# Kernel tuning notes

Measured on AMD Instinct MI355X. Metric: run time of the kernel, lower is better.

Reference implementation:

```python
import jax, jax.numpy as jnp
import numpy as np
import math

DIM = 1024
NUM_HEADS = 16
HEAD_DIM = DIM // NUM_HEADS
MAX_SEQ_LEN = 2048


def setup_inputs() -> dict:
    key = jax.random.key(0)
    ks = jax.random.split(key, 10)
    B, S = 4, 2048
    std = 1.0 / math.sqrt(DIM)
    inp = {
        "x": jax.random.normal(ks[0], (B, S, DIM), dtype=jnp.float32),
        "key_padding_mask": jnp.zeros((B, S), dtype=jnp.bool_),
        "q_w": jax.random.uniform(ks[1], (DIM, DIM), minval=-std, maxval=std),
        "q_b": jax.random.uniform(ks[2], (DIM,), minval=-std, maxval=std),
        "k_w": jax.random.uniform(ks[3], (DIM, DIM), minval=-std, maxval=std),
        "k_b": jax.random.uniform(ks[4], (DIM,), minval=-std, maxval=std),
        "v_w": jax.random.uniform(ks[5], (DIM, DIM), minval=-std, maxval=std),
        "v_b": jax.random.uniform(ks[6], (DIM,), minval=-std, maxval=std),
        "o_w": jax.random.uniform(ks[7], (DIM, DIM), minval=-std, maxval=std),
        "o_b": jax.random.uniform(ks[8], (DIM,), minval=-std, maxval=std),
    }
    return inp


def _rope_tables(seq_len):
    # freqs over half the head dim, per the RotaryPositionalEmbedding module
    half = HEAD_DIM // 2
    freqs = 1.0 / (10000.0 ** (jnp.arange(0, HEAD_DIM, 2, dtype=jnp.float32) / HEAD_DIM))
    pos = jnp.arange(seq_len, dtype=jnp.float32)
    ang = jnp.outer(pos, freqs)  # [S, half]
    return jnp.cos(ang)[:, :half], jnp.sin(ang)[:, :half]


def _apply_rope(t, cos, sin):
    # t: [B, H, S, D]; rotate first/second halves (non-interleaved variant)
    half = HEAD_DIM // 2
    left, right = t[..., :half], t[..., half:]
    return jnp.concatenate([left * cos - right * sin,
                            left * sin + right * cos], axis=-1)


def reference(x, key_padding_mask, q_w, q_b, k_w, k_b, v_w, v_b, o_w, o_b):
    B, S, _ = x.shape
    scale = HEAD_DIM ** -0.5

    def proj(w, b):
        y = jnp.einsum('bsd,ed->bse', x, w) + b  # torch Linear: x @ W^T + b
        return y.reshape(B, S, NUM_HEADS, HEAD_DIM).transpose(0, 2, 1, 3)

    q = proj(q_w, q_b)  # [B, H, S, D]
    k = proj(k_w, k_b)
    v = proj(v_w, v_b)

    cos, sin = _rope_tables(S)  # [S, half], broadcast over B,H
    q = _apply_rope(q, cos, sin)
    k = _apply_rope(k, cos, sin)

    scores = jnp.einsum('bhqd,bhkd->bhqk', q, k) * scale
    scores = jnp.where(key_padding_mask[:, None, None, :], -1e9, scores)
    weights = jax.nn.softmax(scores, axis=-1)  # dropout p=0.0 -> identity
    out = jnp.einsum('bhqk,bhkd->bhqd', weights, v)
    out = out.transpose(0, 2, 1, 3).reshape(B, S, DIM)
    return jnp.einsum('bsd,ed->bse', out, o_w) + o_b
```

## Files before the change

### kernel.cpp

```cpp
#include <hip/hip_runtime.h>
#include <stdint.h>

#define SEQ   2048
#define BATCH 4
#define NH    16
#define HD    64
#define DIMN  1024
#define MROWS (BATCH*SEQ)

typedef __attribute__((ext_vector_type(8))) short          bf16x8;
typedef __attribute__((ext_vector_type(8))) unsigned short ushort8;
typedef __attribute__((ext_vector_type(4))) float          f32x4;

static __device__ __forceinline__ unsigned short f2bf(float f) {
    unsigned int u = __builtin_bit_cast(unsigned int, f);
    u += 0x7fffu + ((u >> 16) & 1u);
    return (unsigned short)(u >> 16);
}
static __device__ __forceinline__ unsigned int pack2bf(float lo, float hi) {
    unsigned int a = __builtin_bit_cast(unsigned int, lo) + 0x8000u;
    unsigned int b = __builtin_bit_cast(unsigned int, hi) + 0x8000u;
    return __builtin_amdgcn_perm(b, a, 0x07060302u);
}
static __device__ __forceinline__ unsigned int pack2bf_trunc(float lo, float hi) {
    return __builtin_amdgcn_perm(__builtin_bit_cast(unsigned int, hi),
                                 __builtin_bit_cast(unsigned int, lo), 0x07060302u);
}

__global__ __launch_bounds__(256) void prologue_kernel(
        const float* __restrict__ x,
        const float* __restrict__ qw, const float* __restrict__ kw,
        const float* __restrict__ vw, const float* __restrict__ ow,
        unsigned short* __restrict__ xb,
        unsigned short* __restrict__ wq, unsigned short* __restrict__ wk,
        unsigned short* __restrict__ wv, unsigned short* __restrict__ wo,
        float* __restrict__ cosT, float* __restrict__ sinT,
        const unsigned char* __restrict__ mask, unsigned long long* __restrict__ m64) {
    const int bx = blockIdx.x, tid = threadIdx.x;
    if (bx < 4096 + 2048) {
        const float* s; unsigned short* d; int i;
        if (bx < 4096) { s = x; d = xb; i = bx * 2048 + tid * 8; }
        else {
            int wb = bx - 4096;
            int wsel = wb >> 9;
            s = wsel == 0 ? qw : (wsel == 1 ? kw : (wsel == 2 ? vw : ow));
            d = wsel == 0 ? wq : (wsel == 1 ? wk : (wsel == 2 ? wv : wo));
            i = (wb & 511) * 2048 + tid * 8;
        }
        float4 a = *(const float4*)(s + i);
        float4 b = *(const float4*)(s + i + 4);
        ushort8 o;
        o[0]=f2bf(a.x); o[1]=f2bf(a.y); o[2]=f2bf(a.z); o[3]=f2bf(a.w);
        o[4]=f2bf(b.x); o[5]=f2bf(b.y); o[6]=f2bf(b.z); o[7]=f2bf(b.w);
        *(ushort8*)(d + i) = o;
    } else if (bx < 6400) {
        int idx = (bx - 6144) * 256 + tid;
        int s = idx >> 5, j = idx & 31;
        float t = (float)(2 * j) / 64.0f;
        float freq = 1.0f / powf(10000.0f, t);
        float ang  = (float)s * freq;
        cosT[idx] = cosf(ang);
        sinT[idx] = sinf(ang);
    } else {
        if (tid < 128) {
            int b = tid >> 5, kt = tid & 31;
            const unsigned char* p = mask + b * SEQ + kt * 64;
            unsigned long long v = 0;
            for (int j = 0; j < 64; j++) v |= (unsigned long long)(p[j] != 0) << j;
            m64[tid] = v;
        }
    }
}

__global__ __launch_bounds__(256) void gemm_qkvt(const unsigned short* __restrict__ X,
        const unsigned short* __restrict__ Wq, const unsigned short* __restrict__ Wk,
        const unsigned short* __restrict__ Wv,
        const float* __restrict__ bq, const float* __restrict__ bk, const float* __restrict__ bv,
        unsigned short* __restrict__ Qo, unsigned short* __restrict__ Ko, unsigned short* __restrict__ Vto,
        const float* __restrict__ cosT, const float* __restrict__ sinT) {
    __shared__ __align__(16) unsigned short As[128 * 32];
    __shared__ __align__(16) unsigned short Bs[128 * 32];
    const int which = blockIdx.x >> 3;
    const int tid  = threadIdx.x;
    const int wid  = tid >> 6, lane = tid & 63;
    const int quad = lane >> 4, l15 = lane & 15;
    const int wm   = wid >> 1,  wn  = wid & 1;

    const unsigned short *Ag, *Bg;
    int m0, n0;
    if (which < 2) {
        m0 = blockIdx.y * 128;
        n0 = (blockIdx.x & 7) * 128;
        Ag = X;  Bg = which == 0 ? Wq : Wk;
    } else {
        m0 = (blockIdx.x & 7) * 128;
        n0 = blockIdx.y * 128;
        Ag = Wv; Bg = X;
    }

    f32x4 acc[4][4];
#pragma unroll
    for (int i = 0; i < 4; i++)
#pragma unroll
        for (int j = 0; j < 4; j++) acc[i][j] = (f32x4)0.0f;

    const int rb = wid * 32 + (lane >> 2);
    const int cb = (((lane & 3) ^ ((lane >> 3) & 3)) * 8);
    const int rq = (quad ^ ((l15 >> 1) & 3)) * 8;

    for (int k0 = 0; k0 < DIMN; k0 += 32) {
#pragma unroll
        for (int i = 0; i < 2; i++) {
            const unsigned short* ga = Ag + (size_t)(m0 + rb + i * 16) * DIMN + k0 + cb;
            __builtin_amdgcn_global_load_lds((const __attribute__((address_space(1))) void*)ga,
                (__attribute__((address_space(3))) void*)&As[(wid * 32 + i * 16) * 32], 16, 0, 0);
            const unsigned short* gb = Bg + (size_t)(n0 + rb + i * 16) * DIMN + k0 + cb;
            __builtin_amdgcn_global_load_lds((const __attribute__((address_space(1))) void*)gb,
                (__attribute__((address_space(3))) void*)&Bs[(wid * 32 + i * 16) * 32], 16, 0, 0);
        }
        __syncthreads();
        bf16x8 af[4], bfr[4];
#pragma unroll
        for (int f = 0; f < 4; f++) af[f]  = *(const bf16x8*)&As[(wm * 64 + f * 16 + l15) * 32 + rq];
#pragma unroll
        for (int f = 0; f < 4; f++) bfr[f] = *(const bf16x8*)&Bs[(wn * 64 + f * 16 + l15) * 32 + rq];
#pragma unroll
        for (int fm = 0; fm < 4; fm++)
#pragma unroll
            for (int fn = 0; fn < 4; fn++)
                acc[fm][fn] = __builtin_amdgcn_mfma_f32_16x16x32_bf16(af[fm], bfr[fn], acc[fm][fn], 0, 0, 0);
        __syncthreads();
    }

    if (which < 2) {
        const float* bias   = which == 0 ? bq : bk;
        unsigned short* Out = which == 0 ? Qo : Ko;
        const float scale = which == 0 ? 0.18033688011112042f : 1.0f;
        float bv4[4];
#pragma unroll
        for (int fn = 0; fn < 4; fn++) bv4[fn] = bias[n0 + wn * 64 + fn * 16 + l15];
        const int h = (n0 >> 6) + wn;
#pragma unroll
        for (int fm = 0; fm < 4; fm++)
#pragma unroll
            for (int r = 0; r < 4; r++) {
                int mrow = m0 + wm * 64 + fm * 16 + quad * 4 + r;
                int b = mrow >> 11, s = mrow & (SEQ - 1);
                unsigned short* orow = Out + ((size_t)(b * NH + h) * SEQ + s) * HD;
                float v0 = (acc[fm][0][r] + bv4[0]) * scale;
                float v1 = (acc[fm][1][r] + bv4[1]) * scale;
                float v2 = (acc[fm][2][r] + bv4[2]) * scale;
                float v3 = (acc[fm][3][r] + bv4[3]) * scale;
                int d0 = l15, d1 = 16 + l15;
                float c0 = cosT[s * 32 + d0], s0 = sinT[s * 32 + d0];
                float c1 = cosT[s * 32 + d1], s1 = sinT[s * 32 + d1];
                orow[d0]      = f2bf(v0 * c0 - v2 * s0);
                orow[d0 + 32] = f2bf(v0 * s0 + v2 * c0);
                orow[d1]      = f2bf(v1 * c1 - v3 * s1);
                orow[d1 + 32] = f2bf(v1 * s1 + v3 * c1);
            }
    } else {
        float4 bb[4];
#pragma unroll
        for (int fm = 0; fm < 4; fm++)
            bb[fm] = *(const float4*)&bv[m0 + wm * 64 + fm * 16 + quad * 4];
        const int b     = n0 >> 11;
        const int sbase = (n0 & (SEQ - 1)) + wn * 64 + l15;
#pragma unroll
        for (int fm = 0; fm < 4; fm++)
#pragma unroll
            for (int r = 0; r < 4; r++) {
                int e = m0 + wm * 64 + fm * 16 + quad * 4 + r;
                float bval = r == 0 ? bb[fm].x : (r == 1 ? bb[fm].y : (r == 2 ? bb[fm].z : bb[fm].w));
                unsigned short* row = Vto + ((size_t)(b * NH + (e >> 6)) * HD + (e & 63)) * SEQ + sbase;
#pragma unroll
                for (int fn = 0; fn < 4; fn++)
                    row[fn * 16] = f2bf(acc[fm][fn][r] + bval);
            }
    }
}

__global__ __launch_bounds__(256) void gemm_bt(const unsigned short* __restrict__ A,
                                               const unsigned short* __restrict__ W,
                                               const float* __restrict__ bias,
                                               float* __restrict__ out) {
    __shared__ __align__(16) unsigned short As[128 * 32];
    __shared__ __align__(16) unsigned short Bs[128 * 32];
    const int tid  = threadIdx.x;
    const int wid  = tid >> 6, lane = tid & 63;
    const int quad = lane >> 4, l15 = lane & 15;
    const int wm   = wid >> 1,  wn  = wid & 1;
    const int m0   = blockIdx.y * 128, n0 = blockIdx.x * 128;

    f32x4 acc[4][4];
#pragma unroll
    for (int i = 0; i < 4; i++)
#pragma unroll
        for (int j = 0; j < 4; j++) acc[i][j] = (f32x4)0.0f;

    const int rb = wid * 32 + (lane >> 2);
    const int cb = (((lane & 3) ^ ((lane >> 3) & 3)) * 8);
    const int rq = (quad ^ ((l15 >> 1) & 3)) * 8;

    for (int k0 = 0; k0 < DIMN; k0 += 32) {
#pragma unroll
        for (int i = 0; i < 2; i++) {
            const unsigned short* ga = A + (size_t)(m0 + rb + i * 16) * DIMN + k0 + cb;
            __builtin_amdgcn_global_load_lds((const __attribute__((address_space(1))) void*)ga,
                (__attribute__((address_space(3))) void*)&As[(wid * 32 + i * 16) * 32], 16, 0, 0);
            const unsigned short* gb = W + (size_t)(n0 + rb + i * 16) * DIMN + k0 + cb;
            __builtin_amdgcn_global_load_lds((const __attribute__((address_space(1))) void*)gb,
                (__attribute__((address_space(3))) void*)&Bs[(wid * 32 + i * 16) * 32], 16, 0, 0);
        }
        __syncthreads();
        bf16x8 af[4], bfr[4];
#pragma unroll
        for (int f = 0; f < 4; f++) af[f]  = *(const bf16x8*)&As[(wm * 64 + f * 16 + l15) * 32 + rq];
#pragma unroll
        for (int f = 0; f < 4; f++) bfr[f] = *(const bf16x8*)&Bs[(wn * 64 + f * 16 + l15) * 32 + rq];
#pragma unroll
        for (int fm = 0; fm < 4; fm++)
#pragma unroll
            for (int fn = 0; fn < 4; fn++)
                acc[fm][fn] = __builtin_amdgcn_mfma_f32_16x16x32_bf16(af[fm], bfr[fn], acc[fm][fn], 0, 0, 0);
        __syncthreads();
    }

    float bv4[4];
#pragma unroll
    for (int fn = 0; fn < 4; fn++) bv4[fn] = bias[n0 + wn * 64 + fn * 16 + l15];
#pragma unroll
    for (int fm = 0; fm < 4; fm++)
#pragma unroll
        for (int r = 0; r < 4; r++) {
            int mrow = m0 + wm * 64 + fm * 16 + quad * 4 + r;
            float* orow = out + (size_t)mrow * DIMN + n0 + wn * 64;
#pragma unroll
            for (int fn = 0; fn < 4; fn++) orow[fn * 16 + l15] = acc[fm][fn][r] + bv4[fn];
        }
}

#define PSTRIDE 36
__global__ __launch_bounds__(256, 4) void attn_kernel(const unsigned short* __restrict__ Q,
                                                      const unsigned short* __restrict__ K,
                                                      const unsigned short* __restrict__ Vt,
                                                      const unsigned long long* __restrict__ M64,
                                                      unsigned short* __restrict__ Ob) {
    __shared__ __align__(16) unsigned short Ks[8 * 512];
    __shared__ __align__(16) unsigned short Vs[8 * 512];
    __shared__ __align__(16) unsigned short Ps[4 * 64 * PSTRIDE];

    const int tid  = threadIdx.x;
    const int wid  = tid >> 6, lane = tid & 63;
    const int quad = lane >> 4, l15 = lane & 15;
    const int bid = blockIdx.x;
    const int bh  = (bid & 7) * 8 + (bid >> 7);
    const int qt  = (bid >> 3) & 15;
    const int b = bh >> 4, h = bh & 15;
    const int q0 = qt * 128;

    bf16x8 qf[2][2];
#pragma unroll
    for (int n = 0; n < 2; n++) {
        const int qs = q0 + wid * 32 + n * 16 + l15;
#pragma unroll
        for (int dk = 0; dk < 2; dk++)
            qf[n][dk] = __builtin_bit_cast(bf16x8,
                *(const uint4*)&Q[((size_t)bh * SEQ + qs) * HD + dk * 32 + quad * 8]);
    }

    f32x4 Oa[4][2];
#pragma unroll
    for (int i = 0; i < 4; i++)
#pragma unroll
        for (int n = 0; n < 2; n++) Oa[i][n] = (f32x4)0.0f;
    float ls[2] = {0.0f, 0.0f};

    unsigned short* Pw = &Ps[wid * 64 * PSTRIDE];
    const unsigned long long* Mrow = M64 + b * (SEQ / 64);

    const int s0 = wid * 2, s1 = s0 + 1;
    const unsigned short* Kg = K + (size_t)bh * SEQ * HD;
    const unsigned short* Vg = Vt + (size_t)bh * HD * SEQ;
    const unsigned short* gk0 = Kg + (size_t)((s0 >> 1) * 16 + l15) * HD + (s0 & 1) * 32 + quad * 8;
    const unsigned short* gk1 = Kg + (size_t)((s1 >> 1) * 16 + l15) * HD + (s1 & 1) * 32 + quad * 8;
    const unsigned short* gv0 = Vg + (size_t)((s0 >> 1) * 16 + l15) * SEQ + (s0 & 1) * 32 + quad * 8;
    const unsigned short* gv1 = Vg + (size_t)((s1 >> 1) * 16 + l15) * SEQ + (s1 & 1) * 32 + quad * 8;

    for (int kt = 0; kt < SEQ / 64; kt++) {
        const int k0 = kt * 64;
        __builtin_amdgcn_global_load_lds(
            (const __attribute__((address_space(1))) void*)(gk0 + (size_t)k0 * HD),
            (__attribute__((address_space(3))) void*)&Ks[s0 * 512], 16, 0, 0);
        __builtin_amdgcn_global_load_lds(
            (const __attribute__((address_space(1))) void*)(gk1 + (size_t)k0 * HD),
            (__attribute__((address_space(3))) void*)&Ks[s1 * 512], 16, 0, 0);
        __builtin_amdgcn_global_load_lds(
            (const __attribute__((address_space(1))) void*)(gv0 + k0),
            (__attribute__((address_space(3))) void*)&Vs[s0 * 512], 16, 0, 0);
        __builtin_amdgcn_global_load_lds(
            (const __attribute__((address_space(1))) void*)(gv1 + k0),
            (__attribute__((address_space(3))) void*)&Vs[s1 * 512], 16, 0, 0);
        unsigned long long mb = Mrow[kt];
        __syncthreads();

#pragma unroll
        for (int h2 = 0; h2 < 2; h2++) {
            bf16x8 kf[2][2];
#pragma unroll
            for (int f2 = 0; f2 < 2; f2++)
#pragma unroll
                for (int dk = 0; dk < 2; dk++)
                    kf[f2][dk] = *(const bf16x8*)&Ks[(((h2 * 2 + f2) << 1) + dk) * 512 + lane * 8];
            bf16x8 vf[4];
#pragma unroll
            for (int df = 0; df < 4; df++)
                vf[df] = *(const bf16x8*)&Vs[((df << 1) + h2) * 512 + lane * 8];

            f32x4 st[2][2];
            __builtin_amdgcn_s_setprio(1);
#pragma unroll
            for (int f2 = 0; f2 < 2; f2++)
#pragma unroll
                for (int n = 0; n < 2; n++) {
                    st[f2][n] = __builtin_amdgcn_mfma_f32_16x16x32_bf16(kf[f2][0], qf[n][0], (f32x4)0.0f, 0, 0, 0);
                    st[f2][n] = __builtin_amdgcn_mfma_f32_16x16x32_bf16(kf[f2][1], qf[n][1], st[f2][n], 0, 0, 0);
                }
            __builtin_amdgcn_s_setprio(0);

            unsigned int mh = (unsigned int)(mb >> (h2 * 32));
            if (mh) {
#pragma unroll
                for (int f2 = 0; f2 < 2; f2++)
#pragma unroll
                    for (int n = 0; n < 2; n++)
#pragma unroll
                        for (int r = 0; r < 4; r++) {
                            int kk = f2 * 16 + quad * 4 + r;
                            if ((mh >> kk) & 1u) st[f2][n][r] = -1e9f;
                        }
            }

#pragma unroll
            for (int f2 = 0; f2 < 2; f2++)
#pragma unroll
                for (int n = 0; n < 2; n++) {
                    float p0 = __builtin_amdgcn_exp2f(st[f2][n][0]);
                    float p1 = __builtin_amdgcn_exp2f(st[f2][n][1]);
                    float p2 = __builtin_amdgcn_exp2f(st[f2][n][2]);
                    float p3 = __builtin_amdgcn_exp2f(st[f2][n][3]);
                    ls[n] += (p0 + p1) + (p2 + p3);
                    uint2 w;
                    w.x = pack2bf_trunc(p0, p1);
                    w.y = pack2bf_trunc(p2, p3);
                    *(uint2*)&Pw[(h2 * 32 + n * 16 + l15) * PSTRIDE + f2 * 16 + quad * 4] = w;
                }
            bf16x8 pf[2];
#pragma unroll
            for (int n = 0; n < 2; n++) {
                uint2 plo = *(const uint2*)&Pw[(h2 * 32 + n * 16 + l15) * PSTRIDE + quad * 8];
                uint2 phi = *(const uint2*)&Pw[(h2 * 32 + n * 16 + l15) * PSTRIDE + quad * 8 + 4];
                uint4 pw4;
                pw4.x = plo.x; pw4.y = plo.y; pw4.z = phi.x; pw4.w = phi.y;
                pf[n] = __builtin_bit_cast(bf16x8, pw4);
            }
            __builtin_amdgcn_s_setprio(1);
#pragma unroll
            for (int df = 0; df < 4; df++)
#pragma unroll
                for (int n = 0; n < 2; n++)
                    Oa[df][n] = __builtin_amdgcn_mfma_f32_16x16x32_bf16(vf[df], pf[n], Oa[df][n], 0, 0, 0);
            __builtin_amdgcn_s_setprio(0);
        }
        __syncthreads();
    }

    float linv[2];
#pragma unroll
    for (int n = 0; n < 2; n++) {
        float l = ls[n];
        l += __shfl_xor(l, 16);
        l += __shfl_xor(l, 32);
        linv[n] = 1.0f / l;
    }

#pragma unroll
    for (int n = 0; n < 2; n++) {
        int s = q0 + wid * 32 + n * 16 + l15;
        unsigned short* orow = Ob + ((size_t)b * SEQ + s) * DIMN + h * HD + quad * 4;
#pragma unroll
        for (int df = 0; df < 4; df++) {
            uint2 w;
            w.x = pack2bf(Oa[df][n][0] * linv[n], Oa[df][n][1] * linv[n]);
            w.y = pack2bf(Oa[df][n][2] * linv[n], Oa[df][n][3] * linv[n]);
            *(uint2*)&orow[df * 16] = w;
        }
    }
}

extern "C" void kernel_launch(void* const* d_in, const int* in_sizes, int n_in,
                              void* d_out, int out_size, void* d_ws, size_t ws_size,
                              hipStream_t stream) {
    (void)in_sizes; (void)n_in; (void)out_size; (void)ws_size;
    const float* x  = (const float*)d_in[0];
    const unsigned char* mask = (const unsigned char*)d_in[1];
    const float* q_w = (const float*)d_in[2];
    const float* q_b = (const float*)d_in[3];
    const float* k_w = (const float*)d_in[4];
    const float* k_b = (const float*)d_in[5];
    const float* v_w = (const float*)d_in[6];
    const float* v_b = (const float*)d_in[7];
    const float* o_w = (const float*)d_in[8];
    const float* o_b = (const float*)d_in[9];
    float* out = (float*)d_out;

    char* w = (char*)d_ws;
    unsigned short* xb = (unsigned short*)w;
    unsigned short* wq = (unsigned short*)(w + (16u << 20));
    unsigned short* wk = wq + (1u << 20);
    unsigned short* wv = wk + (1u << 20);
    unsigned short* wo = wv + (1u << 20);
    float* cosT = (float*)(w + (24u << 20));
    float* sinT = cosT + SEQ * 32;
    unsigned long long* m64 = (unsigned long long*)(w + (24u << 20) + (1u << 19));
    unsigned short* Qb  = (unsigned short*)(w + (25u << 20));
    unsigned short* Kb  = Qb + (8u << 20);
    unsigned short* Vtb = Kb + (8u << 20);
    unsigned short* Ob  = xb;

    prologue_kernel<<<dim3(6401), 256, 0, stream>>>(x, q_w, k_w, v_w, o_w,
                                                    xb, wq, wk, wv, wo,
                                                    cosT, sinT, mask, m64);

    gemm_qkvt<<<dim3(24, 64), 256, 0, stream>>>(xb, wq, wk, wv, q_b, k_b, v_b,
                                                Qb, Kb, Vtb, cosT, sinT);

    attn_kernel<<<dim3(1024), 256, 0, stream>>>(Qb, Kb, Vtb, m64, Ob);

    gemm_bt<<<dim3(DIMN / 128, MROWS / 128), 256, 0, stream>>>(Ob, wo, o_b, out);
}
```

Measured before the change: 283.8 us.

## Double-buffer GEMM LDS tiles and prefetch next K/V tile in attention

Both GEMM kernels now use two LDS buffers per operand, so the global-to-LDS load for the next k-slice is issued before the MFMAs on the current slice run. The attention kernel reads all of the K/V fragments for the tile into registers up front, syncs, then issues the next tile's async loads so they overlap the QK/softmax/PV compute. This is meant to hide global load latency behind MFMA work. In exchange it doubles GEMM LDS use, which may lower occupancy, and raises register pressure in the attention kernel.

```diff
diff --git a/kernel.cpp b/kernel.cpp
--- a/kernel.cpp
+++ b/kernel.cpp
@@ -78,8 +78,10 @@
         const float* __restrict__ bq, const float* __restrict__ bk, const float* __restrict__ bv,
         unsigned short* __restrict__ Qo, unsigned short* __restrict__ Ko, unsigned short* __restrict__ Vto,
         const float* __restrict__ cosT, const float* __restrict__ sinT) {
-    __shared__ __align__(16) unsigned short As[128 * 32];
-    __shared__ __align__(16) unsigned short Bs[128 * 32];
+    __shared__ __align__(16) unsigned short As0[128 * 32];
+    __shared__ __align__(16) unsigned short Bs0[128 * 32];
+    __shared__ __align__(16) unsigned short As1[128 * 32];
+    __shared__ __align__(16) unsigned short Bs1[128 * 32];
     const int which = blockIdx.x >> 3;
     const int tid  = threadIdx.x;
     const int wid  = tid >> 6, lane = tid & 63;
@@ -108,28 +110,38 @@
     const int cb = (((lane & 3) ^ ((lane >> 3) & 3)) * 8);
     const int rq = (quad ^ ((l15 >> 1) & 3)) * 8;
 
-    for (int k0 = 0; k0 < DIMN; k0 += 32) {
-#pragma unroll
-        for (int i = 0; i < 2; i++) {
-            const unsigned short* ga = Ag + (size_t)(m0 + rb + i * 16) * DIMN + k0 + cb;
-            __builtin_amdgcn_global_load_lds((const __attribute__((address_space(1))) void*)ga,
-                (__attribute__((address_space(3))) void*)&As[(wid * 32 + i * 16) * 32], 16, 0, 0);
-            const unsigned short* gb = Bg + (size_t)(n0 + rb + i * 16) * DIMN + k0 + cb;
-            __builtin_amdgcn_global_load_lds((const __attribute__((address_space(1))) void*)gb,
-                (__attribute__((address_space(3))) void*)&Bs[(wid * 32 + i * 16) * 32], 16, 0, 0);
-        }
-        __syncthreads();
-        bf16x8 af[4], bfr[4];
-#pragma unroll
-        for (int f = 0; f < 4; f++) af[f]  = *(const bf16x8*)&As[(wm * 64 + f * 16 + l15) * 32 + rq];
-#pragma unroll
-        for (int f = 0; f < 4; f++) bfr[f] = *(const bf16x8*)&Bs[(wn * 64 + f * 16 + l15) * 32 + rq];
-#pragma unroll
-        for (int fm = 0; fm < 4; fm++)
-#pragma unroll
-            for (int fn = 0; fn < 4; fn++)
-                acc[fm][fn] = __builtin_amdgcn_mfma_f32_16x16x32_bf16(af[fm], bfr[fn], acc[fm][fn], 0, 0, 0);
-        __syncthreads();
+#define GSTAGE(BA, BB, KK) do {                                                             \
+    _Pragma("unroll")                                                                       \
+    for (int i_ = 0; i_ < 2; i_++) {                                                        \
+        const unsigned short* ga_ = Ag + (size_t)(m0 + rb + i_ * 16) * DIMN + (KK) + cb;    \
+        __builtin_amdgcn_global_load_lds((const __attribute__((address_space(1))) void*)ga_,\
+            (__attribute__((address_space(3))) void*)&BA[(wid * 32 + i_ * 16) * 32], 16, 0, 0);\
+        const unsigned short* gb_ = Bg + (size_t)(n0 + rb + i_ * 16) * DIMN + (KK) + cb;    \
+        __builtin_amdgcn_global_load_lds((const __attribute__((address_space(1))) void*)gb_,\
+            (__attribute__((address_space(3))) void*)&BB[(wid * 32 + i_ * 16) * 32], 16, 0, 0);\
+    } } while (0)
+
+#define GCOMP(BA, BB) do {                                                                  \
+    bf16x8 af_[4], bf_[4];                                                                  \
+    _Pragma("unroll")                                                                       \
+    for (int f_ = 0; f_ < 4; f_++) af_[f_] = *(const bf16x8*)&BA[(wm * 64 + f_ * 16 + l15) * 32 + rq]; \
+    _Pragma("unroll")                                                                       \
+    for (int f_ = 0; f_ < 4; f_++) bf_[f_] = *(const bf16x8*)&BB[(wn * 64 + f_ * 16 + l15) * 32 + rq]; \
+    _Pragma("unroll")                                                                       \
+    for (int fm_ = 0; fm_ < 4; fm_++)                                                       \
+        _Pragma("unroll")                                                                   \
+        for (int fn_ = 0; fn_ < 4; fn_++)                                                   \
+            acc[fm_][fn_] = __builtin_amdgcn_mfma_f32_16x16x32_bf16(af_[fm_], bf_[fn_], acc[fm_][fn_], 0, 0, 0); \
+    } while (0)
+
+    GSTAGE(As0, Bs0, 0);
+    for (int k0 = 0; k0 < DIMN; k0 += 64) {
+        __syncthreads();
+        GSTAGE(As1, Bs1, k0 + 32);
+        GCOMP(As0, Bs0);
+        __syncthreads();
+        if (k0 + 64 < DIMN) GSTAGE(As0, Bs0, k0 + 64);
+        GCOMP(As1, Bs1);
     }
 
     if (which < 2) {
@@ -178,14 +190,18 @@
                     row[fn * 16] = f2bf(acc[fm][fn][r] + bval);
             }
     }
+#undef GSTAGE
+#undef GCOMP
 }
 
 __global__ __launch_bounds__(256) void gemm_bt(const unsigned short* __restrict__ A,
                                                const unsigned short* __restrict__ W,
                                                const float* __restrict__ bias,
                                                float* __restrict__ out) {
-    __shared__ __align__(16) unsigned short As[128 * 32];
-    __shared__ __align__(16) unsigned short Bs[128 * 32];
+    __shared__ __align__(16) unsigned short As0[128 * 32];
+    __shared__ __align__(16) unsigned short Bs0[128 * 32];
+    __shared__ __align__(16) unsigned short As1[128 * 32];
+    __shared__ __align__(16) unsigned short Bs1[128 * 32];
     const int tid  = threadIdx.x;
     const int wid  = tid >> 6, lane = tid & 63;
     const int quad = lane >> 4, l15 = lane & 15;
@@ -202,28 +218,38 @@
     const int cb = (((lane & 3) ^ ((lane >> 3) & 3)) * 8);
     const int rq = (quad ^ ((l15 >> 1) & 3)) * 8;
 
-    for (int k0 = 0; k0 < DIMN; k0 += 32) {
-#pragma unroll
-        for (int i = 0; i < 2; i++) {
-            const unsigned short* ga = A + (size_t)(m0 + rb + i * 16) * DIMN + k0 + cb;
-            __builtin_amdgcn_global_load_lds((const __attribute__((address_space(1))) void*)ga,
-                (__attribute__((address_space(3))) void*)&As[(wid * 32 + i * 16) * 32], 16, 0, 0);
-            const unsigned short* gb = W + (size_t)(n0 + rb + i * 16) * DIMN + k0 + cb;
-            __builtin_amdgcn_global_load_lds((const __attribute__((address_space(1))) void*)gb,
-                (__attribute__((address_space(3))) void*)&Bs[(wid * 32 + i * 16) * 32], 16, 0, 0);
-        }
-        __syncthreads();
-        bf16x8 af[4], bfr[4];
-#pragma unroll
-        for (int f = 0; f < 4; f++) af[f]  = *(const bf16x8*)&As[(wm * 64 + f * 16 + l15) * 32 + rq];
-#pragma unroll
-        for (int f = 0; f < 4; f++) bfr[f] = *(const bf16x8*)&Bs[(wn * 64 + f * 16 + l15) * 32 + rq];
-#pragma unroll
-        for (int fm = 0; fm < 4; fm++)
-#pragma unroll
-            for (int fn = 0; fn < 4; fn++)
-                acc[fm][fn] = __builtin_amdgcn_mfma_f32_16x16x32_bf16(af[fm], bfr[fn], acc[fm][fn], 0, 0, 0);
-        __syncthreads();
+#define GSTAGE(BA, BB, KK) do {                                                             \
+    _Pragma("unroll")                                                                       \
+    for (int i_ = 0; i_ < 2; i_++) {                                                        \
+        const unsigned short* ga_ = A + (size_t)(m0 + rb + i_ * 16) * DIMN + (KK) + cb;     \
+        __builtin_amdgcn_global_load_lds((const __attribute__((address_space(1))) void*)ga_,\
+            (__attribute__((address_space(3))) void*)&BA[(wid * 32 + i_ * 16) * 32], 16, 0, 0);\
+        const unsigned short* gb_ = W + (size_t)(n0 + rb + i_ * 16) * DIMN + (KK) + cb;     \
+        __builtin_amdgcn_global_load_lds((const __attribute__((address_space(1))) void*)gb_,\
+            (__attribute__((address_space(3))) void*)&BB[(wid * 32 + i_ * 16) * 32], 16, 0, 0);\
+    } } while (0)
+
+#define GCOMP(BA, BB) do {                                                                  \
+    bf16x8 af_[4], bf_[4];                                                                  \
+    _Pragma("unroll")                                                                       \
+    for (int f_ = 0; f_ < 4; f_++) af_[f_] = *(const bf16x8*)&BA[(wm * 64 + f_ * 16 + l15) * 32 + rq]; \
+    _Pragma("unroll")                                                                       \
+    for (int f_ = 0; f_ < 4; f_++) bf_[f_] = *(const bf16x8*)&BB[(wn * 64 + f_ * 16 + l15) * 32 + rq]; \
+    _Pragma("unroll")                                                                       \
+    for (int fm_ = 0; fm_ < 4; fm_++)                                                       \
+        _Pragma("unroll")                                                                   \
+        for (int fn_ = 0; fn_ < 4; fn_++)                                                   \
+            acc[fm_][fn_] = __builtin_amdgcn_mfma_f32_16x16x32_bf16(af_[fm_], bf_[fn_], acc[fm_][fn_], 0, 0, 0); \
+    } while (0)
+
+    GSTAGE(As0, Bs0, 0);
+    for (int k0 = 0; k0 < DIMN; k0 += 64) {
+        __syncthreads();
+        GSTAGE(As1, Bs1, k0 + 32);
+        GCOMP(As0, Bs0);
+        __syncthreads();
+        if (k0 + 64 < DIMN) GSTAGE(As0, Bs0, k0 + 64);
+        GCOMP(As1, Bs1);
     }
 
     float bv4[4];
@@ -238,6 +264,8 @@
 #pragma unroll
             for (int fn = 0; fn < 4; fn++) orow[fn * 16 + l15] = acc[fm][fn][r] + bv4[fn];
         }
+#undef GSTAGE
+#undef GCOMP
 }
 
 #define PSTRIDE 36
@@ -287,44 +315,51 @@
     const unsigned short* gv0 = Vg + (size_t)((s0 >> 1) * 16 + l15) * SEQ + (s0 & 1) * 32 + quad * 8;
     const unsigned short* gv1 = Vg + (size_t)((s1 >> 1) * 16 + l15) * SEQ + (s1 & 1) * 32 + quad * 8;
 
+#define ASTAGE(K0) do {                                                                  \
+    __builtin_amdgcn_global_load_lds(                                                    \
+        (const __attribute__((address_space(1))) void*)(gk0 + (size_t)(K0) * HD),        \
+        (__attribute__((address_space(3))) void*)&Ks[s0 * 512], 16, 0, 0);               \
+    __builtin_amdgcn_global_load_lds(                                                    \
+        (const __attribute__((address_space(1))) void*)(gk1 + (size_t)(K0) * HD),        \
+        (__attribute__((address_space(3))) void*)&Ks[s1 * 512], 16, 0, 0);               \
+    __builtin_amdgcn_global_load_lds(                                                    \
+        (const __attribute__((address_space(1))) void*)(gv0 + (K0)),                     \
+        (__attribute__((address_space(3))) void*)&Vs[s0 * 512], 16, 0, 0);               \
+    __builtin_amdgcn_global_load_lds(                                                    \
+        (const __attribute__((address_space(1))) void*)(gv1 + (K0)),                     \
+        (__attribute__((address_space(3))) void*)&Vs[s1 * 512], 16, 0, 0);               \
+    } while (0)
+
+    ASTAGE(0);
     for (int kt = 0; kt < SEQ / 64; kt++) {
-        const int k0 = kt * 64;
-        __builtin_amdgcn_global_load_lds(
-            (const __attribute__((address_space(1))) void*)(gk0 + (size_t)k0 * HD),
-            (__attribute__((address_space(3))) void*)&Ks[s0 * 512], 16, 0, 0);
-        __builtin_amdgcn_global_load_lds(
-            (const __attribute__((address_space(1))) void*)(gk1 + (size_t)k0 * HD),
-            (__attribute__((address_space(3))) void*)&Ks[s1 * 512], 16, 0, 0);
-        __builtin_amdgcn_global_load_lds(
-            (const __attribute__((address_space(1))) void*)(gv0 + k0),
-            (__attribute__((address_space(3))) void*)&Vs[s0 * 512], 16, 0, 0);
-        __builtin_amdgcn_global_load_lds(
-            (const __attribute__((address_space(1))) void*)(gv1 + k0),
-            (__attribute__((address_space(3))) void*)&Vs[s1 * 512], 16, 0, 0);
         unsigned long long mb = Mrow[kt];
         __syncthreads();
 
+        bf16x8 kf[2][2][2], vf[2][4];
 #pragma unroll
         for (int h2 = 0; h2 < 2; h2++) {
-            bf16x8 kf[2][2];
 #pragma unroll
             for (int f2 = 0; f2 < 2; f2++)
 #pragma unroll
                 for (int dk = 0; dk < 2; dk++)
-                    kf[f2][dk] = *(const bf16x8*)&Ks[(((h2 * 2 + f2) << 1) + dk) * 512 + lane * 8];
-            bf16x8 vf[4];
+                    kf[h2][f2][dk] = *(const bf16x8*)&Ks[(((h2 * 2 + f2) << 1) + dk) * 512 + lane * 8];
 #pragma unroll
             for (int df = 0; df < 4; df++)
-                vf[df] = *(const bf16x8*)&Vs[((df << 1) + h2) * 512 + lane * 8];
-
+                vf[h2][df] = *(const bf16x8*)&Vs[((df << 1) + h2) * 512 + lane * 8];
+        }
+        __syncthreads();
+        if (kt + 1 < SEQ / 64) ASTAGE((kt + 1) * 64);
+
+#pragma unroll
+        for (int h2 = 0; h2 < 2; h2++) {
             f32x4 st[2][2];
             __builtin_amdgcn_s_setprio(1);
 #pragma unroll
             for (int f2 = 0; f2 < 2; f2++)
 #pragma unroll
                 for (int n = 0; n < 2; n++) {
-                    st[f2][n] = __builtin_amdgcn_mfma_f32_16x16x32_bf16(kf[f2][0], qf[n][0], (f32x4)0.0f, 0, 0, 0);
-                    st[f2][n] = __builtin_amdgcn_mfma_f32_16x16x32_bf16(kf[f2][1], qf[n][1], st[f2][n], 0, 0, 0);
+                    st[f2][n] = __builtin_amdgcn_mfma_f32_16x16x32_bf16(kf[h2][f2][0], qf[n][0], (f32x4)0.0f, 0, 0, 0);
+                    st[f2][n] = __builtin_amdgcn_mfma_f32_16x16x32_bf16(kf[h2][f2][1], qf[n][1], st[f2][n], 0, 0, 0);
                 }
             __builtin_amdgcn_s_setprio(0);
 
@@ -369,11 +404,11 @@
             for (int df = 0; df < 4; df++)
 #pragma unroll
                 for (int n = 0; n < 2; n++)
-                    Oa[df][n] = __builtin_amdgcn_mfma_f32_16x16x32_bf16(vf[df], pf[n], Oa[df][n], 0, 0, 0);
+                    Oa[df][n] = __builtin_amdgcn_mfma_f32_16x16x32_bf16(vf[h2][df], pf[n], Oa[df][n], 0, 0, 0);
             __builtin_amdgcn_s_setprio(0);
         }
-        __syncthreads();
-    }
+    }
+#undef ASTAGE
 
     float linv[2];
 #pragma unroll
```

New measurement: 416.3 us. 1.47x slower.
